# Kernel optimization log

Hardware: AMD Instinct MI355X
Metric: run time of the kernel (lower is better)

The kernel has to match this reference:

```python
import jax, jax.numpy as jnp
import numpy as np

B, S, HID = 2, 2048, 3584
NH, NKV, HD = 16, 8, 256
EPS = 1e-6
SCALING = 256 ** (-0.5)  # query_pre_attn_scalar ** -0.5
NEG = -1e9


def setup_inputs() -> dict:
    key = jax.random.key(0)
    ks = jax.random.split(key, 8)
    hidden_states = jax.random.normal(ks[0], (B, S, HID), jnp.float32)
    # RoPE tables (theta=10000), shape [B, S, HD]
    inv_freq = 1.0 / (10000.0 ** (np.arange(0, HD, 2, dtype=np.float32) / HD))
    pos = np.arange(S, dtype=np.float32)
    freqs = np.outer(pos, inv_freq)                      # [S, HD/2]
    emb = np.concatenate([freqs, freqs], axis=-1)        # [S, HD]
    cos = jnp.broadcast_to(jnp.asarray(np.cos(emb)), (B, S, HD)).astype(jnp.float32)
    sin = jnp.broadcast_to(jnp.asarray(np.sin(emb)), (B, S, HD)).astype(jnp.float32)
    # additive causal mask [B,1,S,S]
    causal = jnp.where(jnp.tril(jnp.ones((S, S), bool)), 0.0, NEG).astype(jnp.float32)
    attention_mask = jnp.broadcast_to(causal[None, None], (B, 1, S, S))
    sc = 0.02
    Wq = jax.random.normal(ks[1], (NH * HD, HID), jnp.float32) * sc
    Wk = jax.random.normal(ks[2], (NKV * HD, HID), jnp.float32) * sc
    Wv = jax.random.normal(ks[3], (NKV * HD, HID), jnp.float32) * sc
    Wo = jax.random.normal(ks[4], (HID, NH * HD), jnp.float32) * sc
    q_norm_w = jax.random.normal(ks[5], (HD,), jnp.float32) * 0.1
    k_norm_w = jax.random.normal(ks[6], (HD,), jnp.float32) * 0.1
    return dict(hidden_states=hidden_states, cos=cos, sin=sin,
                attention_mask=attention_mask, Wq=Wq, Wk=Wk, Wv=Wv, Wo=Wo,
                q_norm_w=q_norm_w, k_norm_w=k_norm_w)


def _rmsnorm(x, w, eps=EPS):
    # out = x * rsqrt(mean(x^2)) * (1 + w)
    xf = x.astype(jnp.float32)
    out = xf * jax.lax.rsqrt(jnp.mean(xf * xf, axis=-1, keepdims=True) + eps)
    return (out * (1.0 + w.astype(jnp.float32))).astype(x.dtype)


def _rotate_half(x):
    d = x.shape[-1] // 2
    return jnp.concatenate([-x[..., d:], x[..., :d]], axis=-1)


def reference(hidden_states, cos, sin, attention_mask, Wq, Wk, Wv, Wo, q_norm_w, k_norm_w):
    b, s, _ = hidden_states.shape
    # projections -> [B, H, S, D]
    q = jnp.einsum('bsh,dh->bsd', hidden_states, Wq).reshape(b, s, NH, HD).transpose(0, 2, 1, 3)
    k = jnp.einsum('bsh,dh->bsd', hidden_states, Wk).reshape(b, s, NKV, HD).transpose(0, 2, 1, 3)
    v = jnp.einsum('bsh,dh->bsd', hidden_states, Wv).reshape(b, s, NKV, HD).transpose(0, 2, 1, 3)
    # per-head RMSNorm on Q/K
    q = _rmsnorm(q, q_norm_w)
    k = _rmsnorm(k, k_norm_w)
    # RoPE, cos/sin broadcast over head dim (unsqueeze_dim=1)
    c, sn = cos[:, None], sin[:, None]
    q = q * c + _rotate_half(q) * sn
    k = k * c + _rotate_half(k) * sn
    # GQA: repeat kv heads (n_rep = NH // NKV)
    n_rep = NH // NKV
    k = jnp.repeat(k, n_rep, axis=1)
    v = jnp.repeat(v, n_rep, axis=1)
    # scaled dot-product attention, softmax in fp32
    scores = jnp.einsum('bhqd,bhkd->bhqk', q, k) * SCALING
    scores = scores + attention_mask[:, :, :, :k.shape[2]]
    attn_weights = jax.nn.softmax(scores.astype(jnp.float32), axis=-1).astype(q.dtype)
    attn_out = jnp.einsum('bhqk,bhkd->bqhd', attn_weights, v).reshape(b, s, NH * HD)
    attn_out = jnp.einsum('bsd,hd->bsh', attn_out, Wo)
    return attn_out, attn_weights
```

## Files before the change

### kernel.cpp

```cpp
#include <hip/hip_runtime.h>

#define B_    2
#define S_    2048
#define HID_  3584
#define NH_   16
#define NKV_  8
#define HD_   256
#define DQ_   (NH_ * HD_)
#define DKV_  (NKV_ * HD_)

static constexpr float SCALE_ = 0.0625f;

typedef __bf16 bf16_t;
typedef __bf16 bf16x8 __attribute__((ext_vector_type(8)));
typedef __bf16 bf16x4 __attribute__((ext_vector_type(4)));
typedef float  f32x4  __attribute__((ext_vector_type(4)));

__global__ __launch_bounds__(256) void cvt_kernel(const float* __restrict__ in,
                                                  bf16_t* __restrict__ out, int n4) {
  int i = blockIdx.x * 256 + threadIdx.x;
  if (i < n4) {
    float4 v = ((const float4*)in)[i];
    bf16x4 o;
    o[0] = (bf16_t)v.x; o[1] = (bf16_t)v.y; o[2] = (bf16_t)v.z; o[3] = (bf16_t)v.w;
    ((bf16x4*)out)[i] = o;
  }
}

__device__ inline void gload_lds16(const bf16_t* g, bf16_t* l) {
  __builtin_amdgcn_global_load_lds(
      (const __attribute__((address_space(1))) void*)g,
      (__attribute__((address_space(3))) void*)l, 16, 0, 0);
}

template<int MODE>
__global__ __launch_bounds__(256) void gemm_lds(const bf16_t* __restrict__ A,
                                                const bf16_t* __restrict__ Bt,
                                                void* __restrict__ outv,
                                                int M, int N, int K, int nh) {
  __shared__ __align__(16) bf16_t As[128 * 64];
  __shared__ __align__(16) bf16_t Bs[128 * 64];
  const int t = threadIdx.x;
  const int lane = t & 63, wv = t >> 6;
  const int wr = wv >> 1, wc = wv & 1;
  const int lr = lane & 15, lg = lane >> 4;
  const size_t m0 = (size_t)blockIdx.y * 128, n0 = (size_t)blockIdx.x * 128;

  const int srow = wv * 32 + (lane >> 3);
  const int scsw = ((lane & 7) ^ ((lane >> 3) & 7)) * 8;
  const bf16_t* ga0 = A  + (m0 + srow) * (size_t)K + scsw;
  const bf16_t* gb0 = Bt + (n0 + srow) * (size_t)K + scsw;

  f32x4 acc[4][4] = {};
  for (int k0 = 0; k0 < K; k0 += 64) {
    __syncthreads();
#pragma unroll
    for (int i = 0; i < 4; ++i) {
      gload_lds16(ga0 + (size_t)(i * 8) * K + k0, &As[(wv * 32 + i * 8) * 64]);
      gload_lds16(gb0 + (size_t)(i * 8) * K + k0, &Bs[(wv * 32 + i * 8) * 64]);
    }
    __syncthreads();

#pragma unroll
    for (int kk = 0; kk < 64; kk += 32) {
      const int c16 = (kk >> 3) + lg;
      const int swz = (c16 ^ (lr & 7)) * 8;
      bf16x8 af[4], bfr[4];
#pragma unroll
      for (int i = 0; i < 4; ++i) af[i]  = *(const bf16x8*)&As[(wr * 64 + i * 16 + lr) * 64 + swz];
#pragma unroll
      for (int j = 0; j < 4; ++j) bfr[j] = *(const bf16x8*)&Bs[(wc * 64 + j * 16 + lr) * 64 + swz];
#pragma unroll
      for (int i = 0; i < 4; ++i)
#pragma unroll
        for (int j = 0; j < 4; ++j)
          acc[i][j] = __builtin_amdgcn_mfma_f32_16x16x32_bf16(af[i], bfr[j], acc[i][j], 0, 0, 0);
    }
  }
#pragma unroll
  for (int i = 0; i < 4; ++i)
#pragma unroll
    for (int j = 0; j < 4; ++j) {
      const int row0 = (int)m0 + wr * 64 + i * 16 + lg * 4;
      const int col  = (int)n0 + wc * 64 + j * 16 + lr;
#pragma unroll
      for (int r = 0; r < 4; ++r) {
        const int row = row0 + r;
        if (MODE == 0) {
          ((float*)outv)[(size_t)row * N + col] = acc[i][j][r];
        } else {
          bf16_t* out = (bf16_t*)outv;
          const bf16_t val = (bf16_t)acc[i][j][r];
          const int b = row >> 11, s = row & (S_ - 1);
          const int h = col >> 8,  hd = col & (HD_ - 1);
          if (MODE == 1) out[((size_t)(b * nh + h) * S_ + s) * HD_ + hd] = val;
          else           out[((size_t)(b * NKV_ + h) * HD_ + hd) * S_ + s] = val;
        }
      }
    }
}

template<int LOGNH>
__global__ __launch_bounds__(256) void normrope_kernel(bf16_t* __restrict__ x,
                                                       const float* __restrict__ w,
                                                       const float* __restrict__ cosb,
                                                       const float* __restrict__ sinb,
                                                       float* __restrict__ rownorm) {
  const int gid  = blockIdx.x * 4 + (threadIdx.x >> 6);
  const int lane = threadIdx.x & 63;
  const int nh = 1 << LOGNH;
  const int h  = gid & (nh - 1);
  const int bs = gid >> LOGNH;
  const int b  = bs >> 11, s = bs & (S_ - 1);
  const int rowi = (b * nh + h) * S_ + s;

  bf16_t* ptr = x + (size_t)rowi * HD_ + lane * 4;
  bf16x4 xv = *(const bf16x4*)ptr;
  float v0 = (float)xv[0], v1 = (float)xv[1], v2 = (float)xv[2], v3 = (float)xv[3];
  float ss = v0 * v0 + v1 * v1 + v2 * v2 + v3 * v3;
#pragma unroll
  for (int off = 1; off < 64; off <<= 1) ss += __shfl_xor(ss, off);
  float r = rsqrtf(ss * (1.0f / HD_) + 1e-6f);

  float4 wv = *(const float4*)(w + lane * 4);
  float x0 = v0 * r * (1.0f + wv.x);
  float x1 = v1 * r * (1.0f + wv.y);
  float x2 = v2 * r * (1.0f + wv.z);
  float x3 = v3 * r * (1.0f + wv.w);

  if (rownorm != nullptr) {
    float s2 = x0 * x0 + x1 * x1 + x2 * x2 + x3 * x3;
#pragma unroll
    for (int off = 1; off < 64; off <<= 1) s2 += __shfl_xor(s2, off);
    if (lane == 0) rownorm[rowi] = s2;
  }

  float p0 = __shfl_xor(x0, 32);
  float p1 = __shfl_xor(x1, 32);
  float p2 = __shfl_xor(x2, 32);
  float p3 = __shfl_xor(x3, 32);
  float sgn = (lane < 32) ? -1.0f : 1.0f;

  float4 c  = *(const float4*)(cosb + (size_t)bs * HD_ + lane * 4);
  float4 sn = *(const float4*)(sinb + (size_t)bs * HD_ + lane * 4);
  bf16x4 o;
  o[0] = (bf16_t)(x0 * c.x + sgn * p0 * sn.x);
  o[1] = (bf16_t)(x1 * c.y + sgn * p1 * sn.y);
  o[2] = (bf16_t)(x2 * c.z + sgn * p2 * sn.z);
  o[3] = (bf16_t)(x3 * c.w + sgn * p3 * sn.w);
  *(bf16x4*)ptr = o;
}

__global__ __launch_bounds__(256) void kmax_reduce_kernel(const float* __restrict__ knorm,
                                                          float* __restrict__ km) {
  __shared__ float red[4];
  const int t = threadIdx.x;
  const float* src = knorm + (size_t)blockIdx.x * S_;
  float m = 0.0f;
  for (int i = t; i < S_; i += 256) m = fmaxf(m, src[i]);
#pragma unroll
  for (int off = 1; off < 64; off <<= 1) m = fmaxf(m, __shfl_xor(m, off));
  if ((t & 63) == 0) red[t >> 6] = m;
  __syncthreads();
  if (t == 0) km[blockIdx.x] = fmaxf(fmaxf(red[0], red[1]), fmaxf(red[2], red[3]));
}

__global__ __launch_bounds__(256) void attn1p_kernel(const bf16_t* __restrict__ qb,
                                                     const bf16_t* __restrict__ kb,
                                                     const bf16_t* __restrict__ vt,
                                                     const float* __restrict__ kmaxbuf,
                                                     float* __restrict__ wout,
                                                     float* __restrict__ linv,
                                                     bf16_t* __restrict__ ctx) {
  __shared__ __align__(16) bf16_t Ks[32][264];
  __shared__ __align__(16) bf16_t Vs[256][40];
  __shared__ __align__(16) bf16_t p_lds[4][16][40];
  __shared__ float qn_lds[4][16];

  const int t = threadIdx.x, w = t >> 6, lane = t & 63;
  const int lr = lane & 15, lg = lane >> 4, rloc = lg * 4;

  const int wgid = blockIdx.x;
  const int g    = ((wgid >> 9) << 3) | (wgid & 7);
  const int idx  = (wgid >> 3) & 63;
  const int b    = g >> 3, kvh = g & 7;
  const int h    = kvh * 2 + (idx >> 5);
  const int qbucket = 31 - (idx & 31);
  const int bh   = b * NH_ + h;
  const int q0b  = qbucket * 64;
  const int q0   = q0b + w * 16;

  const bf16_t* qptr = qb + ((size_t)bh * S_ + q0 + lr) * HD_ + lg * 8;
  bf16x8 qf[8];
#pragma unroll
  for (int c = 0; c < 8; ++c) qf[c] = *(const bf16x8*)(qptr + c * 32);

  float qn = 0.0f;
#pragma unroll
  for (int c = 0; c < 8; ++c)
#pragma unroll
    for (int e = 0; e < 8; ++e) { float v = (float)qf[c][e]; qn += v * v; }
  qn += __shfl_xor(qn, 16);
  qn += __shfl_xor(qn, 32);
  if (lg == 0) qn_lds[w][lr] = qn;
  __syncthreads();
  const float kmax2 = kmaxbuf[b * NKV_ + kvh];
  float mb[4];
#pragma unroll
  for (int r = 0; r < 4; ++r)
    mb[r] = SCALE_ * sqrtf(qn_lds[w][rloc + r] * kmax2) + 1.0f;

  float l[4] = {0.f, 0.f, 0.f, 0.f};
  f32x4 oacc[16] = {};
  const int nkt = (q0b + 64) >> 5;
  float* wrow = wout + ((size_t)bh * S_ + q0) * S_;
  const bf16_t* kgb = kb + (size_t)(b * NKV_ + kvh) * S_ * HD_;
  const bf16_t* vgb = vt + (size_t)(b * NKV_ + kvh) * HD_ * S_;

  const int s_st = t >> 3, c_st = (t & 7) * 32;
  const int vd   = t >> 3, vc   = (t & 7) * 4;
  const int prow = lane >> 2, pcol = (lane & 3) * 8;

  for (int kt = 0; kt < nkt; ++kt) {
    const int colb = kt * 32;
    __syncthreads();
    {
      const bf16_t* src = kgb + (size_t)(colb + s_st) * HD_ + c_st;
      bf16x8 k0 = *(const bf16x8*)(src);
      bf16x8 k1 = *(const bf16x8*)(src + 8);
      bf16x8 k2 = *(const bf16x8*)(src + 16);
      bf16x8 k3 = *(const bf16x8*)(src + 24);
      *(bf16x8*)&Ks[s_st][c_st]      = k0;
      *(bf16x8*)&Ks[s_st][c_st + 8]  = k1;
      *(bf16x8*)&Ks[s_st][c_st + 16] = k2;
      *(bf16x8*)&Ks[s_st][c_st + 24] = k3;
    }
#pragma unroll
    for (int i = 0; i < 8; ++i) {
      const int d = vd + i * 32;
      bf16x4 vv = *(const bf16x4*)(vgb + (size_t)d * S_ + colb + vc);
      *(bf16x4*)&Vs[d][vc] = vv;
    }
    __syncthreads();

    if (colb <= q0 + 15) {
      f32x4 s0 = {0.f, 0.f, 0.f, 0.f}, s1 = {0.f, 0.f, 0.f, 0.f};
#pragma unroll
      for (int c = 0; c < 8; ++c) {
        bf16x8 k0 = *(const bf16x8*)&Ks[lr][c * 32 + lg * 8];
        bf16x8 k1 = *(const bf16x8*)&Ks[16 + lr][c * 32 + lg * 8];
        s0 = __builtin_amdgcn_mfma_f32_16x16x32_bf16(qf[c], k0, s0, 0, 0, 0);
        s1 = __builtin_amdgcn_mfma_f32_16x16x32_bf16(qf[c], k1, s1, 0, 0, 0);
      }
      const int col0 = colb + lr, col1 = col0 + 16;
#pragma unroll
      for (int r = 0; r < 4; ++r) {
        const int row = q0 + rloc + r;
        const float pa = (col0 <= row) ? __expf(s0[r] * SCALE_ - mb[r]) : 0.0f;
        const float pb = (col1 <= row) ? __expf(s1[r] * SCALE_ - mb[r]) : 0.0f;
        l[r] += pa + pb;
        p_lds[w][rloc + r][lr]      = (bf16_t)pa;
        p_lds[w][rloc + r][lr + 16] = (bf16_t)pb;
      }
      bf16x8 pf = *(const bf16x8*)&p_lds[w][lr][lg * 8];
#pragma unroll
      for (int df = 0; df < 16; ++df) {
        bf16x8 vf = *(const bf16x8*)&Vs[df * 16 + lr][lg * 8];
        oacc[df] = __builtin_amdgcn_mfma_f32_16x16x32_bf16(pf, vf, oacc[df], 0, 0, 0);
      }
      {
        bf16x8 pv = *(const bf16x8*)&p_lds[w][prow][pcol];
        float* dst = wrow + (size_t)prow * S_ + colb + pcol;
        f32x4 lo = {(float)pv[0], (float)pv[1], (float)pv[2], (float)pv[3]};
        f32x4 hi = {(float)pv[4], (float)pv[5], (float)pv[6], (float)pv[7]};
        *(f32x4*)dst = lo;
        *(f32x4*)(dst + 4) = hi;
      }
    }
  }
#pragma unroll
  for (int r = 0; r < 4; ++r) {
    l[r] += __shfl_xor(l[r], 1);
    l[r] += __shfl_xor(l[r], 2);
    l[r] += __shfl_xor(l[r], 4);
    l[r] += __shfl_xor(l[r], 8);
  }
  float invl[4];
#pragma unroll
  for (int r = 0; r < 4; ++r) invl[r] = 1.0f / l[r];

  bf16_t* cp = ctx + ((size_t)b * S_ + q0) * DQ_ + h * HD_;
#pragma unroll
  for (int df = 0; df < 16; ++df)
#pragma unroll
    for (int r = 0; r < 4; ++r)
      cp[(size_t)(rloc + r) * DQ_ + df * 16 + lr] = (bf16_t)(oacc[df][r] * invl[r]);

  if (lr == 0) {
#pragma unroll
    for (int r = 0; r < 4; ++r) linv[(size_t)bh * S_ + q0 + rloc + r] = invl[r];
  }
}

__global__ __launch_bounds__(256) void wscale_kernel(float* __restrict__ wbuf,
                                                     const float* __restrict__ linv) {
  const int wv = threadIdx.x >> 6, lane = threadIdx.x & 63;
  const size_t rg = (size_t)blockIdx.x * 4 + wv;
  const int row = (int)(rg & (S_ - 1));
  const float inv = linv[rg];
  float* base = wbuf + rg * S_;
#pragma unroll
  for (int i = 0; i < 8; ++i) {
    const int c0 = (i * 64 + lane) * 4;
    float4 v;
    if (c0 > row) {
      v = make_float4(0.f, 0.f, 0.f, 0.f);
    } else {
      v = *(const float4*)(base + c0);
      v.x = (c0 + 0 <= row) ? v.x * inv : 0.f;
      v.y = (c0 + 1 <= row) ? v.y * inv : 0.f;
      v.z = (c0 + 2 <= row) ? v.z * inv : 0.f;
      v.w = (c0 + 3 <= row) ? v.w * inv : 0.f;
    }
    *(float4*)(base + c0) = v;
  }
}

extern "C" void kernel_launch(void* const* d_in, const int* in_sizes, int n_in,
                              void* d_out, int out_size, void* d_ws, size_t ws_size,
                              hipStream_t stream) {
  const float* hs   = (const float*)d_in[0];
  const float* cosb = (const float*)d_in[1];
  const float* sinb = (const float*)d_in[2];
  const float* Wq = (const float*)d_in[4];
  const float* Wk = (const float*)d_in[5];
  const float* Wv = (const float*)d_in[6];
  const float* Wo = (const float*)d_in[7];
  const float* qw = (const float*)d_in[8];
  const float* kw = (const float*)d_in[9];

  char* ws = (char*)d_ws;
  bf16_t* qb    = (bf16_t*)(ws + 0);
  bf16_t* kb    = (bf16_t*)(ws + 33554432);
  bf16_t* vt    = (bf16_t*)(ws + 50331648);
  bf16_t* ctx   = (bf16_t*)(ws + 67108864);
  float*  linv  = (float*)(ws + 100663296);
  float*  knorm = (float*)(ws + 100925440);
  float*  km    = (float*)(ws + 101056512);
  bf16_t* hsb   = (bf16_t*)(ws + 101056640);
  bf16_t* wqb   = (bf16_t*)(ws + 130416768);
  bf16_t* wkb   = (bf16_t*)(ws + 159776896);
  bf16_t* wvb   = (bf16_t*)(ws + 174456960);
  bf16_t* wob   = (bf16_t*)(ws + 189137024);

  float* out      = (float*)d_out;
  float* attn_out = out;
  float* weights  = out + (size_t)B_ * S_ * HID_;

  const int M = B_ * S_;

  cvt_kernel<<<14336, 256, 0, stream>>>(hs, hsb, (B_ * S_ * HID_) / 4);
  cvt_kernel<<<14336, 256, 0, stream>>>(Wq, wqb, (DQ_ * HID_) / 4);
  cvt_kernel<<<7168,  256, 0, stream>>>(Wk, wkb, (DKV_ * HID_) / 4);
  cvt_kernel<<<7168,  256, 0, stream>>>(Wv, wvb, (DKV_ * HID_) / 4);
  cvt_kernel<<<14336, 256, 0, stream>>>(Wo, wob, (HID_ * DQ_) / 4);

  gemm_lds<1><<<dim3(DQ_ / 128, M / 128), 256, 0, stream>>>(hsb, wqb, qb, M, DQ_, HID_, NH_);
  gemm_lds<1><<<dim3(DKV_ / 128, M / 128), 256, 0, stream>>>(hsb, wkb, kb, M, DKV_, HID_, NKV_);
  gemm_lds<2><<<dim3(DKV_ / 128, M / 128), 256, 0, stream>>>(hsb, wvb, vt, M, DKV_, HID_, NKV_);

  normrope_kernel<4><<<(B_ * S_ * NH_) / 4, 256, 0, stream>>>(qb, qw, cosb, sinb, nullptr);
  normrope_kernel<3><<<(B_ * S_ * NKV_) / 4, 256, 0, stream>>>(kb, kw, cosb, sinb, knorm);
  kmax_reduce_kernel<<<B_ * NKV_, 256, 0, stream>>>(knorm, km);

  attn1p_kernel<<<(S_ / 64) * (B_ * NH_), 256, 0, stream>>>(qb, kb, vt, km, weights, linv, ctx);

  wscale_kernel<<<(B_ * NH_ * S_) / 4, 256, 0, stream>>>(weights, linv);

  gemm_lds<0><<<dim3(HID_ / 128, M / 128), 256, 0, stream>>>(ctx, wob, attn_out, M, HID_, DQ_, 0);
}
```

Before: 990.1 us.

## Use double-buffered 256x256 GEMM tiles and fuse K/V projections

Replaces the 128x128 single-buffered GEMM with a 512-thread 256x256 tile kernel. It double-buffers LDS and issues the next K-slice's global-to-LDS loads in pieces between MFMA groups, so loads overlap compute and each loaded byte is reused more. The K and V projections become one GEMM over the contiguous Wk/Wv buffers, with the epilogue sending columns to either the K layout or the transposed V layout. The trade-offs are 128KB of LDS per block with one block per CU, and only 224-256 blocks per GEMM, which can leave some CUs idle.

New measurement: 986.0 us. Within noise of the previous version (-0.4%).

```diff
diff --git a/kernel.cpp b/kernel.cpp
--- a/kernel.cpp
+++ b/kernel.cpp
@@ -34,54 +34,115 @@
 }
 
 template<int MODE>
-__global__ __launch_bounds__(256) void gemm_lds(const bf16_t* __restrict__ A,
-                                                const bf16_t* __restrict__ Bt,
-                                                void* __restrict__ outv,
-                                                int M, int N, int K, int nh) {
-  __shared__ __align__(16) bf16_t As[128 * 64];
-  __shared__ __align__(16) bf16_t Bs[128 * 64];
+__global__ __launch_bounds__(512, 1) void gemm256(const bf16_t* __restrict__ A,
+                                                  const bf16_t* __restrict__ Bt,
+                                                  void* __restrict__ outv,
+                                                  void* __restrict__ out2v,
+                                                  int M, int N, int K, int nh) {
+  __shared__ __align__(16) bf16_t As[2][256 * 64];
+  __shared__ __align__(16) bf16_t Bs[2][256 * 64];
   const int t = threadIdx.x;
   const int lane = t & 63, wv = t >> 6;
-  const int wr = wv >> 1, wc = wv & 1;
+  const int wr = wv >> 2, wc = wv & 3;
   const int lr = lane & 15, lg = lane >> 4;
-  const size_t m0 = (size_t)blockIdx.y * 128, n0 = (size_t)blockIdx.x * 128;
-
-  const int srow = wv * 32 + (lane >> 3);
-  const int scsw = ((lane & 7) ^ ((lane >> 3) & 7)) * 8;
-  const bf16_t* ga0 = A  + (m0 + srow) * (size_t)K + scsw;
-  const bf16_t* gb0 = Bt + (n0 + srow) * (size_t)K + scsw;
-
-  f32x4 acc[4][4] = {};
-  for (int k0 = 0; k0 < K; k0 += 64) {
+  const size_t m0 = (size_t)blockIdx.y * 256, n0 = (size_t)blockIdx.x * 256;
+
+  const int srow = wv * 8 + (lane >> 3);
+  const int scol = ((lane & 7) ^ ((lane >> 3) & 7)) * 8;
+  const bf16_t* ga = A  + (m0 + srow) * (size_t)K + scol;
+  const bf16_t* gb = Bt + (n0 + srow) * (size_t)K + scol;
+  const int ldso = wv * 512;
+
+#define SITEA(rb, kc, pp) gload_lds16(ga + (size_t)(rb) * K + (kc), &As[pp][(rb) * 64 + ldso])
+#define SITEB(rb, kc, pp) gload_lds16(gb + (size_t)(rb) * K + (kc), &Bs[pp][(rb) * 64 + ldso])
+
+  const int NT = K >> 6;
+  f32x4 acc[8][4] = {};
+  bf16x8 af[4][2], bfr[2][2];
+
+  const int swz0 = ((0 + lg) ^ (lr & 7)) * 8;
+  const int swz1 = ((4 + lg) ^ (lr & 7)) * 8;
+  const int aRB = (wr * 128 + lr) * 64;
+  const int bRB = (wc * 64 + lr) * 64;
+
+  SITEA(0, 0, 0); SITEA(64, 0, 0); SITEA(128, 0, 0); SITEA(192, 0, 0);
+  SITEB(0, 0, 0); SITEB(64, 0, 0); SITEB(128, 0, 0); SITEB(192, 0, 0);
+
+  for (int kt = 0; kt < NT; ++kt) {
+    const int p = kt & 1, q = p ^ 1;
     __syncthreads();
+    const bool st = (kt + 1 < NT);
+    const int kn = (kt + 1) << 6;
+
+    if (st) { SITEA(0, kn, q); SITEA(64, kn, q); }
 #pragma unroll
     for (int i = 0; i < 4; ++i) {
-      gload_lds16(ga0 + (size_t)(i * 8) * K + k0, &As[(wv * 32 + i * 8) * 64]);
-      gload_lds16(gb0 + (size_t)(i * 8) * K + k0, &Bs[(wv * 32 + i * 8) * 64]);
-    }
-    __syncthreads();
-
-#pragma unroll
-    for (int kk = 0; kk < 64; kk += 32) {
-      const int c16 = (kk >> 3) + lg;
-      const int swz = (c16 ^ (lr & 7)) * 8;
-      bf16x8 af[4], bfr[4];
-#pragma unroll
-      for (int i = 0; i < 4; ++i) af[i]  = *(const bf16x8*)&As[(wr * 64 + i * 16 + lr) * 64 + swz];
-#pragma unroll
-      for (int j = 0; j < 4; ++j) bfr[j] = *(const bf16x8*)&Bs[(wc * 64 + j * 16 + lr) * 64 + swz];
-#pragma unroll
-      for (int i = 0; i < 4; ++i)
-#pragma unroll
-        for (int j = 0; j < 4; ++j)
-          acc[i][j] = __builtin_amdgcn_mfma_f32_16x16x32_bf16(af[i], bfr[j], acc[i][j], 0, 0, 0);
-    }
-  }
-#pragma unroll
-  for (int i = 0; i < 4; ++i)
+      af[i][0] = *(const bf16x8*)&As[p][aRB + i * 1024 + swz0];
+      af[i][1] = *(const bf16x8*)&As[p][aRB + i * 1024 + swz1];
+    }
+#pragma unroll
+    for (int j = 0; j < 2; ++j) {
+      bfr[j][0] = *(const bf16x8*)&Bs[p][bRB + j * 1024 + swz0];
+      bfr[j][1] = *(const bf16x8*)&Bs[p][bRB + j * 1024 + swz1];
+    }
+#pragma unroll
+    for (int i = 0; i < 4; ++i)
+#pragma unroll
+      for (int j = 0; j < 2; ++j) {
+        acc[i][j] = __builtin_amdgcn_mfma_f32_16x16x32_bf16(af[i][0], bfr[j][0], acc[i][j], 0, 0, 0);
+        acc[i][j] = __builtin_amdgcn_mfma_f32_16x16x32_bf16(af[i][1], bfr[j][1], acc[i][j], 0, 0, 0);
+      }
+
+    if (st) { SITEA(128, kn, q); SITEA(192, kn, q); }
+#pragma unroll
+    for (int i = 0; i < 4; ++i) {
+      af[i][0] = *(const bf16x8*)&As[p][aRB + (i + 4) * 1024 + swz0];
+      af[i][1] = *(const bf16x8*)&As[p][aRB + (i + 4) * 1024 + swz1];
+    }
+#pragma unroll
+    for (int i = 0; i < 4; ++i)
+#pragma unroll
+      for (int j = 0; j < 2; ++j) {
+        acc[i + 4][j] = __builtin_amdgcn_mfma_f32_16x16x32_bf16(af[i][0], bfr[j][0], acc[i + 4][j], 0, 0, 0);
+        acc[i + 4][j] = __builtin_amdgcn_mfma_f32_16x16x32_bf16(af[i][1], bfr[j][1], acc[i + 4][j], 0, 0, 0);
+      }
+
+    if (st) { SITEB(0, kn, q); SITEB(64, kn, q); }
+#pragma unroll
+    for (int j = 0; j < 2; ++j) {
+      bfr[j][0] = *(const bf16x8*)&Bs[p][bRB + (j + 2) * 1024 + swz0];
+      bfr[j][1] = *(const bf16x8*)&Bs[p][bRB + (j + 2) * 1024 + swz1];
+    }
+#pragma unroll
+    for (int i = 0; i < 4; ++i)
+#pragma unroll
+      for (int j = 0; j < 2; ++j) {
+        acc[i + 4][j + 2] = __builtin_amdgcn_mfma_f32_16x16x32_bf16(af[i][0], bfr[j][0], acc[i + 4][j + 2], 0, 0, 0);
+        acc[i + 4][j + 2] = __builtin_amdgcn_mfma_f32_16x16x32_bf16(af[i][1], bfr[j][1], acc[i + 4][j + 2], 0, 0, 0);
+      }
+
+    if (st) { SITEB(128, kn, q); SITEB(192, kn, q); }
+#pragma unroll
+    for (int i = 0; i < 4; ++i) {
+      af[i][0] = *(const bf16x8*)&As[p][aRB + i * 1024 + swz0];
+      af[i][1] = *(const bf16x8*)&As[p][aRB + i * 1024 + swz1];
+    }
+#pragma unroll
+    for (int i = 0; i < 4; ++i)
+#pragma unroll
+      for (int j = 0; j < 2; ++j) {
+        acc[i][j + 2] = __builtin_amdgcn_mfma_f32_16x16x32_bf16(af[i][0], bfr[j][0], acc[i][j + 2], 0, 0, 0);
+        acc[i][j + 2] = __builtin_amdgcn_mfma_f32_16x16x32_bf16(af[i][1], bfr[j][1], acc[i][j + 2], 0, 0, 0);
+      }
+  }
+#undef SITEA
+#undef SITEB
+
+#pragma unroll
+  for (int i = 0; i < 8; ++i)
 #pragma unroll
     for (int j = 0; j < 4; ++j) {
-      const int row0 = (int)m0 + wr * 64 + i * 16 + lg * 4;
+      const int row0 = (int)m0 + wr * 128 + i * 16 + lg * 4;
       const int col  = (int)n0 + wc * 64 + j * 16 + lr;
 #pragma unroll
       for (int r = 0; r < 4; ++r) {
@@ -89,12 +150,21 @@
         if (MODE == 0) {
           ((float*)outv)[(size_t)row * N + col] = acc[i][j][r];
         } else {
-          bf16_t* out = (bf16_t*)outv;
           const bf16_t val = (bf16_t)acc[i][j][r];
           const int b = row >> 11, s = row & (S_ - 1);
-          const int h = col >> 8,  hd = col & (HD_ - 1);
-          if (MODE == 1) out[((size_t)(b * nh + h) * S_ + s) * HD_ + hd] = val;
-          else           out[((size_t)(b * NKV_ + h) * HD_ + hd) * S_ + s] = val;
+          if (MODE == 1) {
+            const int h = col >> 8, hd = col & (HD_ - 1);
+            ((bf16_t*)outv)[((size_t)(b * nh + h) * S_ + s) * HD_ + hd] = val;
+          } else {
+            if (col < DKV_) {
+              const int h = col >> 8, hd = col & (HD_ - 1);
+              ((bf16_t*)outv)[((size_t)(b * NKV_ + h) * S_ + s) * HD_ + hd] = val;
+            } else {
+              const int c2 = col - DKV_;
+              const int h = c2 >> 8, hd = c2 & (HD_ - 1);
+              ((bf16_t*)out2v)[((size_t)(b * NKV_ + h) * HD_ + hd) * S_ + s] = val;
+            }
+          }
         }
       }
     }
@@ -365,9 +435,8 @@
   cvt_kernel<<<7168,  256, 0, stream>>>(Wv, wvb, (DKV_ * HID_) / 4);
   cvt_kernel<<<14336, 256, 0, stream>>>(Wo, wob, (HID_ * DQ_) / 4);
 
-  gemm_lds<1><<<dim3(DQ_ / 128, M / 128), 256, 0, stream>>>(hsb, wqb, qb, M, DQ_, HID_, NH_);
-  gemm_lds<1><<<dim3(DKV_ / 128, M / 128), 256, 0, stream>>>(hsb, wkb, kb, M, DKV_, HID_, NKV_);
-  gemm_lds<2><<<dim3(DKV_ / 128, M / 128), 256, 0, stream>>>(hsb, wvb, vt, M, DKV_, HID_, NKV_);
+  gemm256<1><<<dim3(DQ_ / 256, M / 256), 512, 0, stream>>>(hsb, wqb, qb, nullptr, M, DQ_, HID_, NH_);
+  gemm256<3><<<dim3((2 * DKV_) / 256, M / 256), 512, 0, stream>>>(hsb, wkb, kb, vt, M, 2 * DKV_, HID_, NKV_);
 
   normrope_kernel<4><<<(B_ * S_ * NH_) / 4, 256, 0, stream>>>(qb, qw, cosb, sinb, nullptr);
   normrope_kernel<3><<<(B_ * S_ * NKV_) / 4, 256, 0, stream>>>(kb, kw, cosb, sinb, knorm);
@@ -377,5 +446,5 @@
 
   wscale_kernel<<<(B_ * NH_ * S_) / 4, 256, 0, stream>>>(weights, linv);
 
-  gemm_lds<0><<<dim3(HID_ / 128, M / 128), 256, 0, stream>>>(ctx, wob, attn_out, M, HID_, DQ_, 0);
-}
+  gemm256<0><<<dim3(HID_ / 256, M / 256), 512, 0, stream>>>(ctx, wob, attn_out, nullptr, M, HID_, DQ_, 0);
+}
```
